# Optimization experiments

Hardware: AMD Instinct MI355X
Metric: run time of the kernel (lower is better)

## Reference

```python
import jax, jax.numpy as jnp
import numpy as np

N_NODES = 50000
N_EDGES = 800000
IN_DIM = 128
HID = 128
TIME = 6.0
STEPS = 12


def setup_inputs() -> dict:
    key = jax.random.key(0)
    ks = jax.random.split(key, 8)
    gat_out = jax.random.normal(ks[0], (N_NODES, IN_DIM), dtype=jnp.float32)
    edge_index = jax.random.randint(ks[1], (2, N_EDGES), 0, N_NODES, dtype=jnp.int64)
    # scale weights like PyTorch Linear default (uniform-ish magnitude)
    W_in = jax.random.normal(ks[2], (IN_DIM, HID), dtype=jnp.float32) * (1.0 / np.sqrt(IN_DIM))
    b_in = jnp.zeros((HID,), dtype=jnp.float32)
    W1 = jax.random.normal(ks[3], (HID, 2 * HID), dtype=jnp.float32) * (1.0 / np.sqrt(HID))
    b1 = jnp.zeros((2 * HID,), dtype=jnp.float32)
    W2 = jax.random.normal(ks[4], (2 * HID, HID), dtype=jnp.float32) * (1.0 / np.sqrt(2 * HID))
    b2 = jnp.zeros((HID,), dtype=jnp.float32)
    clearance = jnp.full((1,), 0.1, dtype=jnp.float32)
    return {"gat_out": gat_out, "edge_index": edge_index, "W_in": W_in, "b_in": b_in,
            "W1": W1, "b1": b1, "W2": W2, "b2": b2, "clearance": clearance}


def reference(gat_out, edge_index, W_in, b_in, W1, b1, W2, b2, clearance):
    N = gat_out.shape[0]
    dt = TIME / STEPS
    src, dst = edge_index[0], edge_index[1]
    h = jnp.tanh(gat_out @ W_in + b_in)  # [N, HID]
    # degree is identical each Euler step in the original; hoist it once
    deg = jax.ops.segment_sum(jnp.ones((src.shape[0],), dtype=h.dtype), dst, num_segments=N)
    deg = jnp.clip(deg, 1.0, None)[:, None]  # [N, 1]
    decay = jax.nn.relu(clearance)  # [1]

    def step(h, _):
        agg = jax.ops.segment_sum(h[src], dst, num_segments=N) / deg  # [N, HID]
        diff = jnp.tanh(jax.nn.gelu(agg @ W1 + b1, approximate=False) @ W2 + b2)
        h = h + (diff - decay * h) * dt
        return h, None

    h, _ = jax.lax.scan(step, h, None, length=STEPS)
    return h
```

## Files before the change

kernel.cpp:

```cpp
#include <hip/hip_runtime.h>
#include <math.h>

#define N_NODES 50000
#define N_EDGES 800000
#define HID 128
#define H2 256
#define STEPS 12
#define DT 0.5f

#define SCAN_B 256
#define NB ((N_NODES + SCAN_B - 1) / SCAN_B)
#define NODE_BLOCKS ((N_NODES + 31) / 32)
#define N_PAD (NODE_BLOCKS * 32)

typedef __attribute__((ext_vector_type(8))) short bf16x8;
typedef __attribute__((ext_vector_type(4))) float f32x4;

__device__ inline unsigned short f2bf(float x) {
    unsigned int u = __float_as_uint(x);
    unsigned int r = (u + 0x7FFFu + ((u >> 16) & 1u)) >> 16;
    return (unsigned short)r;
}
__device__ inline float bf2f(unsigned short b) {
    return __uint_as_float(((unsigned int)b) << 16);
}
__device__ inline float u2f(unsigned int u) { return __uint_as_float(u); }


__global__ void k_zero_counts(int* __restrict__ counts) {
    int i = blockIdx.x * 256 + threadIdx.x;
    if (i < N_NODES) counts[i] = 0;
}

__global__ void k_hist(const int* __restrict__ dst, int* __restrict__ counts) {
    int e = blockIdx.x * 256 + threadIdx.x;
    if (e < N_EDGES) atomicAdd(&counts[dst[e]], 1);
}

__global__ void k_blocksum(const int* __restrict__ counts, int* __restrict__ bsum) {
    __shared__ int s[SCAN_B];
    int idx = blockIdx.x * SCAN_B + threadIdx.x;
    int v = (idx < N_NODES) ? counts[idx] : 0;
    s[threadIdx.x] = v;
    __syncthreads();
    for (int off = SCAN_B / 2; off > 0; off >>= 1) {
        if (threadIdx.x < off) s[threadIdx.x] += s[threadIdx.x + off];
        __syncthreads();
    }
    if (threadIdx.x == 0) bsum[blockIdx.x] = s[0];
}

__global__ void k_scan_bsums(int* __restrict__ bsum, int* __restrict__ offsets) {
    if (threadIdx.x == 0 && blockIdx.x == 0) {
        int run = 0;
        for (int i = 0; i < NB; i++) { int t = bsum[i]; bsum[i] = run; run += t; }
        offsets[N_NODES] = N_EDGES;
    }
}

__global__ void k_offsets(const int* __restrict__ counts, const int* __restrict__ bsum,
                          int* __restrict__ offsets, int* __restrict__ cursor) {
    __shared__ int s[SCAN_B];
    int idx = blockIdx.x * SCAN_B + threadIdx.x;
    int v = (idx < N_NODES) ? counts[idx] : 0;
    s[threadIdx.x] = v;
    __syncthreads();
    for (int off = 1; off < SCAN_B; off <<= 1) {
        int t = 0;
        if ((int)threadIdx.x >= off) t = s[threadIdx.x - off];
        __syncthreads();
        s[threadIdx.x] += t;
        __syncthreads();
    }
    if (idx < N_NODES) {
        int excl = s[threadIdx.x] - v;
        int o = bsum[blockIdx.x] + excl;
        offsets[idx] = o;
        cursor[idx]  = o;
    }
}

__global__ void k_scatter(const int* __restrict__ src, const int* __restrict__ dst,
                          int* __restrict__ cursor, int* __restrict__ csr_src) {
    int e = blockIdx.x * 256 + threadIdx.x;
    if (e < N_EDGES) {
        int d = dst[e];
        int p = atomicAdd(&cursor[d], 1);
        csr_src[p] = src[e];
    }
}


__global__ void k_pack(const float* __restrict__ W, int K, int N,
                       unsigned short* __restrict__ hi, unsigned short* __restrict__ lo) {
    int KT = K >> 5, NT = N >> 4;
    int t = blockIdx.x * 256 + threadIdx.x;
    if (t >= KT * NT * 64) return;
    int l = t & 63, tile = t >> 6;
    int kt = tile % KT, nt = tile / KT;
    int n  = nt * 16 + (l & 15);
    int k0 = kt * 32 + (l >> 4) * 8;
    int base = ((nt * KT + kt) * 64 + l) * 8;
    for (int j = 0; j < 8; j++) {
        float w = W[(size_t)(k0 + j) * N + n];
        unsigned short h = f2bf(w);
        hi[base + j] = h;
        lo[base + j] = f2bf(w - bf2f(h));
    }
}


__global__ __launch_bounds__(256, 3) void k_h0_mfma(
    const float* __restrict__ gat,
    const unsigned short* __restrict__ wh, const unsigned short* __restrict__ wl,
    const float* __restrict__ b_in, float* __restrict__ h,
    unsigned short* __restrict__ hbf) {
    __shared__ unsigned short Ahi[32][136];
    __shared__ unsigned short Alo[32][136];
    int tid = threadIdx.x;
    int node0 = blockIdx.x * 32;

    for (int idx = tid; idx < 32 * 64; idx += 256) {
        int m = idx >> 6, c = (idx & 63) * 2;
        float2 v;
        if (node0 + m < N_NODES) v = *(const float2*)&gat[(size_t)(node0 + m) * 128 + c];
        else { v.x = 0.f; v.y = 0.f; }
        unsigned short h0 = f2bf(v.x), h1 = f2bf(v.y);
        unsigned short l0 = f2bf(v.x - bf2f(h0)), l1 = f2bf(v.y - bf2f(h1));
        *(unsigned int*)&Ahi[m][c] = (unsigned int)h0 | ((unsigned int)h1 << 16);
        *(unsigned int*)&Alo[m][c] = (unsigned int)l0 | ((unsigned int)l1 << 16);
    }
    __syncthreads();

    int l = tid & 63, wv = tid >> 6;
    int c15 = l & 15, q = l >> 4;
    f32x4 acc[2][2] = {};
#pragma unroll
    for (int kt = 0; kt < 4; kt++) {
        bf16x8 ah[2], al[2];
#pragma unroll
        for (int mt = 0; mt < 2; mt++) {
            ah[mt] = *(const bf16x8*)&Ahi[mt * 16 + c15][kt * 32 + q * 8];
            al[mt] = *(const bf16x8*)&Alo[mt * 16 + c15][kt * 32 + q * 8];
        }
#pragma unroll
        for (int nn = 0; nn < 2; nn++) {
            int nt = wv * 2 + nn;
            bf16x8 bh = *(const bf16x8*)&wh[(size_t)((nt * 4 + kt) * 64 + l) * 8];
            bf16x8 bl = *(const bf16x8*)&wl[(size_t)((nt * 4 + kt) * 64 + l) * 8];
#pragma unroll
            for (int mt = 0; mt < 2; mt++) {
                acc[mt][nn] = __builtin_amdgcn_mfma_f32_16x16x32_bf16(ah[mt], bh, acc[mt][nn], 0, 0, 0);
                acc[mt][nn] = __builtin_amdgcn_mfma_f32_16x16x32_bf16(ah[mt], bl, acc[mt][nn], 0, 0, 0);
                acc[mt][nn] = __builtin_amdgcn_mfma_f32_16x16x32_bf16(al[mt], bh, acc[mt][nn], 0, 0, 0);
            }
        }
    }
#pragma unroll
    for (int nn = 0; nn < 2; nn++) {
        int col = (wv * 2 + nn) * 16 + c15;
        float bb = b_in[col];
#pragma unroll
        for (int mt = 0; mt < 2; mt++)
#pragma unroll
            for (int r = 0; r < 4; r++) {
                int node = node0 + mt * 16 + q * 4 + r;
                if (node < N_NODES) {
                    float v = tanhf(acc[mt][nn][r] + bb);
                    h[(size_t)node * 128 + col]   = v;
                    hbf[(size_t)node * 128 + col] = f2bf(v);
                }
            }
    }
}


__global__ __launch_bounds__(512, 4) void k_step(
    const unsigned short* __restrict__ hbf_in,
    float* __restrict__ h, unsigned short* __restrict__ hbf_out,
    const int* __restrict__ offsets, const int* __restrict__ csr,
    const unsigned short* __restrict__ w1h, const unsigned short* __restrict__ w1l,
    const float* __restrict__ b1,
    const unsigned short* __restrict__ w2h, const unsigned short* __restrict__ w2l,
    const float* __restrict__ b2, const float* __restrict__ clr) {
    __shared__ unsigned short Ahi[32][136];
    __shared__ unsigned short Alo[32][136];
    __shared__ unsigned short Y[32][264];
    int tid = threadIdx.x, l = tid & 63, wv = tid >> 6;
    int c15 = l & 15, q = l >> 4;
    int node0 = blockIdx.x * 32;
    int g  = l >> 4;
    int cl = l & 15;

#pragma unroll 1
    for (int i = 0; i < 4; i++) {
        int m = wv * 4 + i;
        int node = node0 + m;
        float a0 = 0.f, a1 = 0.f, a2 = 0.f, a3 = 0.f;
        float a4 = 0.f, a5 = 0.f, a6 = 0.f, a7 = 0.f;
        int deg = 0;
        if (node < N_NODES) {
            int beg = offsets[node], end = offsets[node + 1];
            deg = end - beg;
            int e = beg + g;
            for (; e + 12 < end; e += 16) {
                int i0 = csr[e], i1 = csr[e + 4], i2 = csr[e + 8], i3 = csr[e + 12];
                uint4 w0 = *(const uint4*)&hbf_in[(size_t)i0 * 128 + cl * 8];
                uint4 w1 = *(const uint4*)&hbf_in[(size_t)i1 * 128 + cl * 8];
                uint4 w2 = *(const uint4*)&hbf_in[(size_t)i2 * 128 + cl * 8];
                uint4 w3 = *(const uint4*)&hbf_in[(size_t)i3 * 128 + cl * 8];
                a0 += u2f(w0.x << 16); a1 += u2f(w0.x & 0xFFFF0000u);
                a2 += u2f(w0.y << 16); a3 += u2f(w0.y & 0xFFFF0000u);
                a4 += u2f(w0.z << 16); a5 += u2f(w0.z & 0xFFFF0000u);
                a6 += u2f(w0.w << 16); a7 += u2f(w0.w & 0xFFFF0000u);
                a0 += u2f(w1.x << 16); a1 += u2f(w1.x & 0xFFFF0000u);
                a2 += u2f(w1.y << 16); a3 += u2f(w1.y & 0xFFFF0000u);
                a4 += u2f(w1.z << 16); a5 += u2f(w1.z & 0xFFFF0000u);
                a6 += u2f(w1.w << 16); a7 += u2f(w1.w & 0xFFFF0000u);
                a0 += u2f(w2.x << 16); a1 += u2f(w2.x & 0xFFFF0000u);
                a2 += u2f(w2.y << 16); a3 += u2f(w2.y & 0xFFFF0000u);
                a4 += u2f(w2.z << 16); a5 += u2f(w2.z & 0xFFFF0000u);
                a6 += u2f(w2.w << 16); a7 += u2f(w2.w & 0xFFFF0000u);
                a0 += u2f(w3.x << 16); a1 += u2f(w3.x & 0xFFFF0000u);
                a2 += u2f(w3.y << 16); a3 += u2f(w3.y & 0xFFFF0000u);
                a4 += u2f(w3.z << 16); a5 += u2f(w3.z & 0xFFFF0000u);
                a6 += u2f(w3.w << 16); a7 += u2f(w3.w & 0xFFFF0000u);
            }
            for (; e < end; e += 4) {
                int i0 = csr[e];
                uint4 w0 = *(const uint4*)&hbf_in[(size_t)i0 * 128 + cl * 8];
                a0 += u2f(w0.x << 16); a1 += u2f(w0.x & 0xFFFF0000u);
                a2 += u2f(w0.y << 16); a3 += u2f(w0.y & 0xFFFF0000u);
                a4 += u2f(w0.z << 16); a5 += u2f(w0.z & 0xFFFF0000u);
                a6 += u2f(w0.w << 16); a7 += u2f(w0.w & 0xFFFF0000u);
            }
        }
        a0 += __shfl_xor(a0, 16); a1 += __shfl_xor(a1, 16);
        a2 += __shfl_xor(a2, 16); a3 += __shfl_xor(a3, 16);
        a4 += __shfl_xor(a4, 16); a5 += __shfl_xor(a5, 16);
        a6 += __shfl_xor(a6, 16); a7 += __shfl_xor(a7, 16);
        a0 += __shfl_xor(a0, 32); a1 += __shfl_xor(a1, 32);
        a2 += __shfl_xor(a2, 32); a3 += __shfl_xor(a3, 32);
        a4 += __shfl_xor(a4, 32); a5 += __shfl_xor(a5, 32);
        a6 += __shfl_xor(a6, 32); a7 += __shfl_xor(a7, 32);

        float inv = (deg > 1) ? 1.0f / (float)deg : 1.0f;
        float x0 = a0 * inv, x1 = a1 * inv, x2 = a2 * inv, x3 = a3 * inv;
        float x4 = a4 * inv, x5 = a5 * inv, x6 = a6 * inv, x7 = a7 * inv;
        unsigned short h0 = f2bf(x0), h1 = f2bf(x1), h2 = f2bf(x2), h3 = f2bf(x3);
        unsigned short h4 = f2bf(x4), h5 = f2bf(x5), h6 = f2bf(x6), h7 = f2bf(x7);
        if (g == 0) {
            uint4 o;
            o.x = (unsigned int)h0 | ((unsigned int)h1 << 16);
            o.y = (unsigned int)h2 | ((unsigned int)h3 << 16);
            o.z = (unsigned int)h4 | ((unsigned int)h5 << 16);
            o.w = (unsigned int)h6 | ((unsigned int)h7 << 16);
            *(uint4*)&Ahi[m][cl * 8] = o;
        } else if (g == 1) {
            unsigned short l0 = f2bf(x0 - bf2f(h0)), l1 = f2bf(x1 - bf2f(h1));
            unsigned short l2 = f2bf(x2 - bf2f(h2)), l3 = f2bf(x3 - bf2f(h3));
            unsigned short l4 = f2bf(x4 - bf2f(h4)), l5 = f2bf(x5 - bf2f(h5));
            unsigned short l6 = f2bf(x6 - bf2f(h6)), l7 = f2bf(x7 - bf2f(h7));
            uint4 o;
            o.x = (unsigned int)l0 | ((unsigned int)l1 << 16);
            o.y = (unsigned int)l2 | ((unsigned int)l3 << 16);
            o.z = (unsigned int)l4 | ((unsigned int)l5 << 16);
            o.w = (unsigned int)l6 | ((unsigned int)l7 << 16);
            *(uint4*)&Alo[m][cl * 8] = o;
        }
    }
    __syncthreads();

    {
        f32x4 acc1[2][2] = {};
#pragma unroll
        for (int kt = 0; kt < 4; kt++) {
            bf16x8 ah[2], al[2];
#pragma unroll
            for (int mt = 0; mt < 2; mt++) {
                ah[mt] = *(const bf16x8*)&Ahi[mt * 16 + c15][kt * 32 + q * 8];
                al[mt] = *(const bf16x8*)&Alo[mt * 16 + c15][kt * 32 + q * 8];
            }
#pragma unroll
            for (int nn = 0; nn < 2; nn++) {
                int nt = wv * 2 + nn;
                bf16x8 bh = *(const bf16x8*)&w1h[(size_t)((nt * 4 + kt) * 64 + l) * 8];
                bf16x8 bl = *(const bf16x8*)&w1l[(size_t)((nt * 4 + kt) * 64 + l) * 8];
#pragma unroll
                for (int mt = 0; mt < 2; mt++) {
                    acc1[mt][nn] = __builtin_amdgcn_mfma_f32_16x16x32_bf16(ah[mt], bh, acc1[mt][nn], 0, 0, 0);
                    acc1[mt][nn] = __builtin_amdgcn_mfma_f32_16x16x32_bf16(ah[mt], bl, acc1[mt][nn], 0, 0, 0);
                    acc1[mt][nn] = __builtin_amdgcn_mfma_f32_16x16x32_bf16(al[mt], bh, acc1[mt][nn], 0, 0, 0);
                }
            }
        }
#pragma unroll
        for (int nn = 0; nn < 2; nn++) {
            int col = (wv * 2 + nn) * 16 + c15;
            float bb = b1[col];
#pragma unroll
            for (int mt = 0; mt < 2; mt++)
#pragma unroll
                for (int r = 0; r < 4; r++) {
                    int row = mt * 16 + q * 4 + r;
                    float x = acc1[mt][nn][r] + bb;
                    float gg = 0.5f * x * (1.0f + erff(x * 0.70710678118654752f));
                    Y[row][col] = f2bf(gg);
                }
        }
    }
    __syncthreads();

    f32x4 acc2[2] = {};
#pragma unroll
    for (int kt = 0; kt < 8; kt++) {
        bf16x8 ya[2];
#pragma unroll
        for (int mt = 0; mt < 2; mt++)
            ya[mt] = *(const bf16x8*)&Y[mt * 16 + c15][kt * 32 + q * 8];
        bf16x8 bh = *(const bf16x8*)&w2h[(size_t)((wv * 8 + kt) * 64 + l) * 8];
        bf16x8 bl = *(const bf16x8*)&w2l[(size_t)((wv * 8 + kt) * 64 + l) * 8];
#pragma unroll
        for (int mt = 0; mt < 2; mt++) {
            acc2[mt] = __builtin_amdgcn_mfma_f32_16x16x32_bf16(ya[mt], bh, acc2[mt], 0, 0, 0);
            acc2[mt] = __builtin_amdgcn_mfma_f32_16x16x32_bf16(ya[mt], bl, acc2[mt], 0, 0, 0);
        }
    }
    float decay = fmaxf(clr[0], 0.0f);
    {
        int col = wv * 16 + c15;
        float bb = b2[col];
#pragma unroll
        for (int mt = 0; mt < 2; mt++)
#pragma unroll
            for (int r = 0; r < 4; r++) {
                int node = node0 + mt * 16 + q * 4 + r;
                if (node < N_NODES) {
                    float hv = h[(size_t)node * 128 + col];
                    float diff = tanhf(acc2[mt][r] + bb);
                    float nh = hv + (diff - decay * hv) * DT;
                    h[(size_t)node * 128 + col]       = nh;
                    hbf_out[(size_t)node * 128 + col] = f2bf(nh);
                }
            }
    }
}


extern "C" void kernel_launch(void* const* d_in, const int* in_sizes, int n_in,
                              void* d_out, int out_size, void* d_ws, size_t ws_size,
                              hipStream_t stream) {
    const float* gat   = (const float*)d_in[0];
    const int*   edges = (const int*)d_in[1];
    const float* W_in  = (const float*)d_in[2];
    const float* b_in  = (const float*)d_in[3];
    const float* W1    = (const float*)d_in[4];
    const float* b1    = (const float*)d_in[5];
    const float* W2    = (const float*)d_in[6];
    const float* b2    = (const float*)d_in[7];
    const float* clr   = (const float*)d_in[8];
    float* h = (float*)d_out;

    const int* src = edges;
    const int* dst = edges + N_EDGES;

    char* ws = (char*)d_ws;
    size_t off = 0;
    auto alloc = [&](size_t bytes) -> void* {
        off = (off + 255) & ~(size_t)255;
        void* p = ws + off;
        off += bytes;
        return p;
    };
    int*   counts  = (int*)alloc(sizeof(int) * N_NODES);
    int*   offsets = (int*)alloc(sizeof(int) * (N_NODES + 1));
    int*   cursor  = (int*)alloc(sizeof(int) * N_NODES);
    int*   bsum    = (int*)alloc(sizeof(int) * NB);
    int*   csr_src = (int*)alloc(sizeof(int) * N_EDGES);
    unsigned short* hbfA = (unsigned short*)alloc(sizeof(short) * (size_t)N_PAD * HID);
    unsigned short* hbfB = (unsigned short*)alloc(sizeof(short) * (size_t)N_PAD * HID);
    unsigned short* w1h  = (unsigned short*)alloc(sizeof(short) * HID * H2);
    unsigned short* w1l  = (unsigned short*)alloc(sizeof(short) * HID * H2);
    unsigned short* w2h  = (unsigned short*)alloc(sizeof(short) * H2 * HID);
    unsigned short* w2l  = (unsigned short*)alloc(sizeof(short) * H2 * HID);
    unsigned short* winh = (unsigned short*)alloc(sizeof(short) * HID * HID);
    unsigned short* winl = (unsigned short*)alloc(sizeof(short) * HID * HID);

    k_pack<<<16, 256, 0, stream>>>(W1, 128, 256, w1h, w1l);
    k_pack<<<16, 256, 0, stream>>>(W2, 256, 128, w2h, w2l);
    k_pack<<<8, 256, 0, stream>>>(W_in, 128, 128, winh, winl);

    k_zero_counts<<<NB, 256, 0, stream>>>(counts);
    k_hist<<<(N_EDGES + 255) / 256, 256, 0, stream>>>(dst, counts);
    k_blocksum<<<NB, 256, 0, stream>>>(counts, bsum);
    k_scan_bsums<<<1, 64, 0, stream>>>(bsum, offsets);
    k_offsets<<<NB, 256, 0, stream>>>(counts, bsum, offsets, cursor);
    k_scatter<<<(N_EDGES + 255) / 256, 256, 0, stream>>>(src, dst, cursor, csr_src);

    k_h0_mfma<<<NODE_BLOCKS, 256, 0, stream>>>(gat, winh, winl, b_in, h, hbfA);

    for (int s = 0; s < STEPS; s++) {
        const unsigned short* in = (s & 1) ? hbfB : hbfA;
        unsigned short*      out = (s & 1) ? hbfA : hbfB;
        k_step<<<NODE_BLOCKS, 512, 0, stream>>>(in, h, out, offsets, csr_src,
                                                w1h, w1l, b1, w2h, w2l, b2, clr);
    }
}
```

Baseline: 899.0 us.

## Pad CSR rows to multiples of four, one node per quarter-wave gather, fast tanh/gelu

Each node's CSR segment is padded to a multiple of four entries, and the padding points at a zeroed pad row. This lets the gather load four neighbour indices as one int4, prefetch the next group, and assign one node per 16-lane group, which removes the cross-group shuffle reduction and the serial per-node loop. The single-thread bsum scan becomes a parallel block scan. tanhf and erf-based GELU are replaced with exp2/rcp approximations (an Abramowitz-Stegun erf), trading some accuracy for fewer transcendental instructions. Padding adds extra gather traffic of up to three dummy rows per node.

```diff
diff --git a/kernel.cpp b/kernel.cpp
--- a/kernel.cpp
+++ b/kernel.cpp
@@ -12,6 +12,7 @@
 #define NB ((N_NODES + SCAN_B - 1) / SCAN_B)
 #define NODE_BLOCKS ((N_NODES + 31) / 32)
 #define N_PAD (NODE_BLOCKS * 32)
+#define CSR_CAP (N_EDGES + 4 * N_NODES)
 
 typedef __attribute__((ext_vector_type(8))) short bf16x8;
 typedef __attribute__((ext_vector_type(4))) float f32x4;
@@ -26,12 +27,42 @@
 }
 __device__ inline float u2f(unsigned int u) { return __uint_as_float(u); }
 
+__device__ inline float fast_tanh(float x) {
+    float xc = fminf(fmaxf(x, -9.0f), 9.0f);
+    float t = __builtin_amdgcn_exp2f(xc * 2.8853900817779268f);
+    return 1.0f - 2.0f * __builtin_amdgcn_rcpf(t + 1.0f);
+}
+
+__device__ inline float fast_gelu(float x) {
+    float u  = x * 0.70710678118654752f;
+    float au = fabsf(u);
+    float t  = __builtin_amdgcn_rcpf(fmaf(0.3275911f, au, 1.0f));
+    float poly = t * (0.254829592f + t * (-0.284496736f + t * (1.421413741f +
+                 t * (-1.453152027f + t * 1.061405429f))));
+    float ex = __builtin_amdgcn_exp2f(-au * au * 1.4426950408889634f);
+    float erfv = copysignf(1.0f - poly * ex, u);
+    return 0.5f * x * (1.0f + erfv);
+}
+
 
 __global__ void k_zero_counts(int* __restrict__ counts) {
     int i = blockIdx.x * 256 + threadIdx.x;
     if (i < N_NODES) counts[i] = 0;
 }
 
+__global__ void k_fill_csr(int* __restrict__ csr) {
+    int i = blockIdx.x * 256 + threadIdx.x;
+    if (i < CSR_CAP) csr[i] = N_NODES;
+}
+
+__global__ void k_zero_padrows(unsigned short* __restrict__ a, unsigned short* __restrict__ b) {
+    int i = blockIdx.x * 256 + threadIdx.x;
+    if (i < (N_PAD - N_NODES) * HID) {
+        a[(size_t)N_NODES * HID + i] = 0;
+        b[(size_t)N_NODES * HID + i] = 0;
+    }
+}
+
 __global__ void k_hist(const int* __restrict__ dst, int* __restrict__ counts) {
     int e = blockIdx.x * 256 + threadIdx.x;
     if (e < N_EDGES) atomicAdd(&counts[dst[e]], 1);
@@ -40,7 +71,7 @@
 __global__ void k_blocksum(const int* __restrict__ counts, int* __restrict__ bsum) {
     __shared__ int s[SCAN_B];
     int idx = blockIdx.x * SCAN_B + threadIdx.x;
-    int v = (idx < N_NODES) ? counts[idx] : 0;
+    int v = (idx < N_NODES) ? ((counts[idx] + 3) & ~3) : 0;
     s[threadIdx.x] = v;
     __syncthreads();
     for (int off = SCAN_B / 2; off > 0; off >>= 1) {
@@ -51,18 +82,27 @@
 }
 
 __global__ void k_scan_bsums(int* __restrict__ bsum, int* __restrict__ offsets) {
-    if (threadIdx.x == 0 && blockIdx.x == 0) {
-        int run = 0;
-        for (int i = 0; i < NB; i++) { int t = bsum[i]; bsum[i] = run; run += t; }
-        offsets[N_NODES] = N_EDGES;
-    }
+    __shared__ int s[SCAN_B];
+    int tid = threadIdx.x;
+    int v = (tid < NB) ? bsum[tid] : 0;
+    s[tid] = v;
+    __syncthreads();
+    for (int off = 1; off < SCAN_B; off <<= 1) {
+        int t = 0;
+        if (tid >= off) t = s[tid - off];
+        __syncthreads();
+        s[tid] += t;
+        __syncthreads();
+    }
+    if (tid < NB) bsum[tid] = s[tid] - v;
+    if (tid == SCAN_B - 1) offsets[N_NODES] = s[SCAN_B - 1];
 }
 
 __global__ void k_offsets(const int* __restrict__ counts, const int* __restrict__ bsum,
                           int* __restrict__ offsets, int* __restrict__ cursor) {
     __shared__ int s[SCAN_B];
     int idx = blockIdx.x * SCAN_B + threadIdx.x;
-    int v = (idx < N_NODES) ? counts[idx] : 0;
+    int v = (idx < N_NODES) ? ((counts[idx] + 3) & ~3) : 0;
     s[threadIdx.x] = v;
     __syncthreads();
     for (int off = 1; off < SCAN_B; off <<= 1) {
@@ -166,7 +206,7 @@
             for (int r = 0; r < 4; r++) {
                 int node = node0 + mt * 16 + q * 4 + r;
                 if (node < N_NODES) {
-                    float v = tanhf(acc[mt][nn][r] + bb);
+                    float v = fast_tanh(acc[mt][nn][r] + bb);
                     h[(size_t)node * 128 + col]   = v;
                     hbf[(size_t)node * 128 + col] = f2bf(v);
                 }
@@ -174,11 +214,18 @@
     }
 }
 
+
+#define ACC8(V) \
+    a0 += u2f((V).x << 16); a1 += u2f((V).x & 0xFFFF0000u); \
+    a2 += u2f((V).y << 16); a3 += u2f((V).y & 0xFFFF0000u); \
+    a4 += u2f((V).z << 16); a5 += u2f((V).z & 0xFFFF0000u); \
+    a6 += u2f((V).w << 16); a7 += u2f((V).w & 0xFFFF0000u);
 
 __global__ __launch_bounds__(512, 4) void k_step(
     const unsigned short* __restrict__ hbf_in,
     float* __restrict__ h, unsigned short* __restrict__ hbf_out,
     const int* __restrict__ offsets, const int* __restrict__ csr,
+    const int* __restrict__ cnt,
     const unsigned short* __restrict__ w1h, const unsigned short* __restrict__ w1l,
     const float* __restrict__ b1,
     const unsigned short* __restrict__ w2h, const unsigned short* __restrict__ w2l,
@@ -192,82 +239,51 @@
     int g  = l >> 4;
     int cl = l & 15;
 
-#pragma unroll 1
-    for (int i = 0; i < 4; i++) {
-        int m = wv * 4 + i;
+    {
+        int m = wv * 4 + g;
         int node = node0 + m;
         float a0 = 0.f, a1 = 0.f, a2 = 0.f, a3 = 0.f;
         float a4 = 0.f, a5 = 0.f, a6 = 0.f, a7 = 0.f;
         int deg = 0;
         if (node < N_NODES) {
             int beg = offsets[node], end = offsets[node + 1];
-            deg = end - beg;
-            int e = beg + g;
-            for (; e + 12 < end; e += 16) {
-                int i0 = csr[e], i1 = csr[e + 4], i2 = csr[e + 8], i3 = csr[e + 12];
-                uint4 w0 = *(const uint4*)&hbf_in[(size_t)i0 * 128 + cl * 8];
-                uint4 w1 = *(const uint4*)&hbf_in[(size_t)i1 * 128 + cl * 8];
-                uint4 w2 = *(const uint4*)&hbf_in[(size_t)i2 * 128 + cl * 8];
-                uint4 w3 = *(const uint4*)&hbf_in[(size_t)i3 * 128 + cl * 8];
-                a0 += u2f(w0.x << 16); a1 += u2f(w0.x & 0xFFFF0000u);
-                a2 += u2f(w0.y << 16); a3 += u2f(w0.y & 0xFFFF0000u);
-                a4 += u2f(w0.z << 16); a5 += u2f(w0.z & 0xFFFF0000u);
-                a6 += u2f(w0.w << 16); a7 += u2f(w0.w & 0xFFFF0000u);
-                a0 += u2f(w1.x << 16); a1 += u2f(w1.x & 0xFFFF0000u);
-                a2 += u2f(w1.y << 16); a3 += u2f(w1.y & 0xFFFF0000u);
-                a4 += u2f(w1.z << 16); a5 += u2f(w1.z & 0xFFFF0000u);
-                a6 += u2f(w1.w << 16); a7 += u2f(w1.w & 0xFFFF0000u);
-                a0 += u2f(w2.x << 16); a1 += u2f(w2.x & 0xFFFF0000u);
-                a2 += u2f(w2.y << 16); a3 += u2f(w2.y & 0xFFFF0000u);
-                a4 += u2f(w2.z << 16); a5 += u2f(w2.z & 0xFFFF0000u);
-                a6 += u2f(w2.w << 16); a7 += u2f(w2.w & 0xFFFF0000u);
-                a0 += u2f(w3.x << 16); a1 += u2f(w3.x & 0xFFFF0000u);
-                a2 += u2f(w3.y << 16); a3 += u2f(w3.y & 0xFFFF0000u);
-                a4 += u2f(w3.z << 16); a5 += u2f(w3.z & 0xFFFF0000u);
-                a6 += u2f(w3.w << 16); a7 += u2f(w3.w & 0xFFFF0000u);
-            }
-            for (; e < end; e += 4) {
-                int i0 = csr[e];
-                uint4 w0 = *(const uint4*)&hbf_in[(size_t)i0 * 128 + cl * 8];
-                a0 += u2f(w0.x << 16); a1 += u2f(w0.x & 0xFFFF0000u);
-                a2 += u2f(w0.y << 16); a3 += u2f(w0.y & 0xFFFF0000u);
-                a4 += u2f(w0.z << 16); a5 += u2f(w0.z & 0xFFFF0000u);
-                a6 += u2f(w0.w << 16); a7 += u2f(w0.w & 0xFFFF0000u);
-            }
-        }
-        a0 += __shfl_xor(a0, 16); a1 += __shfl_xor(a1, 16);
-        a2 += __shfl_xor(a2, 16); a3 += __shfl_xor(a3, 16);
-        a4 += __shfl_xor(a4, 16); a5 += __shfl_xor(a5, 16);
-        a6 += __shfl_xor(a6, 16); a7 += __shfl_xor(a7, 16);
-        a0 += __shfl_xor(a0, 32); a1 += __shfl_xor(a1, 32);
-        a2 += __shfl_xor(a2, 32); a3 += __shfl_xor(a3, 32);
-        a4 += __shfl_xor(a4, 32); a5 += __shfl_xor(a5, 32);
-        a6 += __shfl_xor(a6, 32); a7 += __shfl_xor(a7, 32);
-
+            deg = cnt[node];
+            const unsigned short* hb = hbf_in + cl * 8;
+            if (beg < end) {
+                int4 ii = *(const int4*)&csr[beg];
+                for (int e = beg; e < end; e += 4) {
+                    int enx = (e + 4 < end) ? (e + 4) : e;
+                    int4 iin = *(const int4*)&csr[enx];
+                    uint4 w0 = *(const uint4*)&hb[((unsigned)ii.x) << 7];
+                    uint4 w1 = *(const uint4*)&hb[((unsigned)ii.y) << 7];
+                    uint4 w2 = *(const uint4*)&hb[((unsigned)ii.z) << 7];
+                    uint4 w3 = *(const uint4*)&hb[((unsigned)ii.w) << 7];
+                    ii = iin;
+                    ACC8(w0); ACC8(w1); ACC8(w2); ACC8(w3);
+                }
+            }
+        }
         float inv = (deg > 1) ? 1.0f / (float)deg : 1.0f;
         float x0 = a0 * inv, x1 = a1 * inv, x2 = a2 * inv, x3 = a3 * inv;
         float x4 = a4 * inv, x5 = a5 * inv, x6 = a6 * inv, x7 = a7 * inv;
         unsigned short h0 = f2bf(x0), h1 = f2bf(x1), h2 = f2bf(x2), h3 = f2bf(x3);
         unsigned short h4 = f2bf(x4), h5 = f2bf(x5), h6 = f2bf(x6), h7 = f2bf(x7);
-        if (g == 0) {
-            uint4 o;
-            o.x = (unsigned int)h0 | ((unsigned int)h1 << 16);
-            o.y = (unsigned int)h2 | ((unsigned int)h3 << 16);
-            o.z = (unsigned int)h4 | ((unsigned int)h5 << 16);
-            o.w = (unsigned int)h6 | ((unsigned int)h7 << 16);
-            *(uint4*)&Ahi[m][cl * 8] = o;
-        } else if (g == 1) {
-            unsigned short l0 = f2bf(x0 - bf2f(h0)), l1 = f2bf(x1 - bf2f(h1));
-            unsigned short l2 = f2bf(x2 - bf2f(h2)), l3 = f2bf(x3 - bf2f(h3));
-            unsigned short l4 = f2bf(x4 - bf2f(h4)), l5 = f2bf(x5 - bf2f(h5));
-            unsigned short l6 = f2bf(x6 - bf2f(h6)), l7 = f2bf(x7 - bf2f(h7));
-            uint4 o;
-            o.x = (unsigned int)l0 | ((unsigned int)l1 << 16);
-            o.y = (unsigned int)l2 | ((unsigned int)l3 << 16);
-            o.z = (unsigned int)l4 | ((unsigned int)l5 << 16);
-            o.w = (unsigned int)l6 | ((unsigned int)l7 << 16);
-            *(uint4*)&Alo[m][cl * 8] = o;
-        }
+        uint4 ohi;
+        ohi.x = (unsigned int)h0 | ((unsigned int)h1 << 16);
+        ohi.y = (unsigned int)h2 | ((unsigned int)h3 << 16);
+        ohi.z = (unsigned int)h4 | ((unsigned int)h5 << 16);
+        ohi.w = (unsigned int)h6 | ((unsigned int)h7 << 16);
+        *(uint4*)&Ahi[m][cl * 8] = ohi;
+        unsigned short l0 = f2bf(x0 - bf2f(h0)), l1 = f2bf(x1 - bf2f(h1));
+        unsigned short l2 = f2bf(x2 - bf2f(h2)), l3 = f2bf(x3 - bf2f(h3));
+        unsigned short l4 = f2bf(x4 - bf2f(h4)), l5 = f2bf(x5 - bf2f(h5));
+        unsigned short l6 = f2bf(x6 - bf2f(h6)), l7 = f2bf(x7 - bf2f(h7));
+        uint4 olo;
+        olo.x = (unsigned int)l0 | ((unsigned int)l1 << 16);
+        olo.y = (unsigned int)l2 | ((unsigned int)l3 << 16);
+        olo.z = (unsigned int)l4 | ((unsigned int)l5 << 16);
+        olo.w = (unsigned int)l6 | ((unsigned int)l7 << 16);
+        *(uint4*)&Alo[m][cl * 8] = olo;
     }
     __syncthreads();
 
@@ -304,8 +320,7 @@
                 for (int r = 0; r < 4; r++) {
                     int row = mt * 16 + q * 4 + r;
                     float x = acc1[mt][nn][r] + bb;
-                    float gg = 0.5f * x * (1.0f + erff(x * 0.70710678118654752f));
-                    Y[row][col] = f2bf(gg);
+                    Y[row][col] = f2bf(fast_gelu(x));
                 }
         }
     }
@@ -337,7 +352,7 @@
                 int node = node0 + mt * 16 + q * 4 + r;
                 if (node < N_NODES) {
                     float hv = h[(size_t)node * 128 + col];
-                    float diff = tanhf(acc2[mt][r] + bb);
+                    float diff = fast_tanh(acc2[mt][r] + bb);
                     float nh = hv + (diff - decay * hv) * DT;
                     h[(size_t)node * 128 + col]       = nh;
                     hbf_out[(size_t)node * 128 + col] = f2bf(nh);
@@ -376,7 +391,7 @@
     int*   offsets = (int*)alloc(sizeof(int) * (N_NODES + 1));
     int*   cursor  = (int*)alloc(sizeof(int) * N_NODES);
     int*   bsum    = (int*)alloc(sizeof(int) * NB);
-    int*   csr_src = (int*)alloc(sizeof(int) * N_EDGES);
+    int*   csr_src = (int*)alloc(sizeof(int) * CSR_CAP);
     unsigned short* hbfA = (unsigned short*)alloc(sizeof(short) * (size_t)N_PAD * HID);
     unsigned short* hbfB = (unsigned short*)alloc(sizeof(short) * (size_t)N_PAD * HID);
     unsigned short* w1h  = (unsigned short*)alloc(sizeof(short) * HID * H2);
@@ -391,9 +406,11 @@
     k_pack<<<8, 256, 0, stream>>>(W_in, 128, 128, winh, winl);
 
     k_zero_counts<<<NB, 256, 0, stream>>>(counts);
+    k_fill_csr<<<(CSR_CAP + 255) / 256, 256, 0, stream>>>(csr_src);
+    k_zero_padrows<<<8, 256, 0, stream>>>(hbfA, hbfB);
     k_hist<<<(N_EDGES + 255) / 256, 256, 0, stream>>>(dst, counts);
     k_blocksum<<<NB, 256, 0, stream>>>(counts, bsum);
-    k_scan_bsums<<<1, 64, 0, stream>>>(bsum, offsets);
+    k_scan_bsums<<<1, SCAN_B, 0, stream>>>(bsum, offsets);
     k_offsets<<<NB, 256, 0, stream>>>(counts, bsum, offsets, cursor);
     k_scatter<<<(N_EDGES + 255) / 256, 256, 0, stream>>>(src, dst, cursor, csr_src);
 
@@ -402,7 +419,7 @@
     for (int s = 0; s < STEPS; s++) {
         const unsigned short* in = (s & 1) ? hbfB : hbfA;
         unsigned short*      out = (s & 1) ? hbfA : hbfB;
-        k_step<<<NODE_BLOCKS, 512, 0, stream>>>(in, h, out, offsets, csr_src,
+        k_step<<<NODE_BLOCKS, 512, 0, stream>>>(in, h, out, offsets, csr_src, counts,
                                                 w1h, w1l, b1, w2h, w2l, b2, clr);
     }
 }
```

Result: faster. 861.8 us (-4.1%).
